# Performance work log

Measured on AMD Instinct MI355X. Metric: run time of the kernel, lower is better.

Reference implementation:

```python
import jax, jax.numpy as jnp
import numpy as np

B, T, D, L, K = 4, 2048, 2048, 2048, 4  # batch, seq, width, lru_width, conv temporal width


def setup_inputs() -> dict:
    key = jax.random.key(0)
    ks = jax.random.split(key, 12)
    s = 0.02
    f32 = jnp.float32
    return {
        "x": jax.random.normal(ks[0], (B, T, D), f32),
        "w_y": jax.random.normal(ks[1], (D, L), f32) * s,
        "b_y": jnp.zeros((L,), f32),
        "w_x": jax.random.normal(ks[2], (D, L), f32) * s,
        "b_x": jnp.zeros((L,), f32),
        "conv_w": jax.random.normal(ks[3], (K, L), f32) * s,
        "conv_b": jnp.zeros((L,), f32),
        "a_param": jax.random.uniform(ks[4], (L,), f32, 0.5, 4.0),
        "w_ig": jax.random.normal(ks[5], (L, L), f32) * s,
        "b_ig": jnp.zeros((L,), f32),
        "w_ag": jax.random.normal(ks[6], (L, L), f32) * s,
        "b_ag": jnp.zeros((L,), f32),
        "w_out": jax.random.normal(ks[7], (L, D), f32) * s,
        "b_out": jnp.zeros((D,), f32),
    }


def reference(x, w_y, b_y, w_x, b_x, conv_w, conv_b, a_param,
              w_ig, b_ig, w_ag, b_ag, w_out, b_out):
    # x: [B, T, D] (batch_first=True)
    Tn = x.shape[1]
    # gate branch: GELU(linear_y(x))
    y = jax.nn.gelu(jnp.einsum('btd,dl->btl', x, w_y) + b_y, approximate=False)
    # recurrent branch: linear_x -> causal depthwise conv1d (width K)
    xb = jnp.einsum('btd,dl->btl', x, w_x) + b_x
    xp = jnp.pad(xb, ((0, 0), (K - 1, 0), (0, 0)))  # zero left pad (fresh cache)
    conv = conv_b
    for k in range(K):  # y_t = b + sum_k w[k] * x_{t-(K-1-k)}
        conv = conv + conv_w[k] * xp[:, k:k + Tn]
    # RG-LRU
    gate_x = jax.nn.sigmoid(jnp.einsum('btl,lm->btm', conv, w_ig) + b_ig)
    gate_a = jax.nn.sigmoid(jnp.einsum('btl,lm->btm', conv, w_ag) + b_ag)
    log_a = -8.0 * gate_a * jax.nn.softplus(a_param)  # [B,T,L]
    a = jnp.exp(log_a)
    mult = jnp.sqrt(1.0 - jnp.exp(2.0 * log_a))
    reset = (jnp.arange(Tn) == 0)[None, :, None]  # reset at sequence start
    a = jnp.where(reset, 0.0, a)
    mult = jnp.where(reset, 1.0, mult)
    nx = gate_x * conv * mult
    # linear diagonal scan h_t = a_t * h_{t-1} + nx_t
    def step(h, inp):
        a_t, x_t = inp
        h = a_t * h + x_t
        return h, h
    h0 = jnp.zeros((x.shape[0], a.shape[-1]), x.dtype)
    hn, hs = jax.lax.scan(step, h0, (a.transpose(1, 0, 2), nx.transpose(1, 0, 2)))
    h_seq = hs.transpose(1, 0, 2)  # [B,T,L]
    out = jnp.einsum('btl,ld->btd', h_seq * y, w_out) + b_out
    return out, hn
```

## Files before the change

kernel.cpp:

```cpp
#include <hip/hip_runtime.h>
#include <math.h>

#define B_ 4
#define T_ 2048
#define D_ 2048
#define L_ 2048
#define KW 4
#define M_ (B_*T_)

typedef unsigned short u16;
typedef unsigned short u16x8 __attribute__((ext_vector_type(8)));
typedef __bf16 bf16x8 __attribute__((ext_vector_type(8)));
typedef float f32x4 __attribute__((ext_vector_type(4)));

__device__ __forceinline__ u16 f2bf(float f) {
    unsigned u = __float_as_uint(f);
    u += 0x7fffu + ((u >> 16) & 1u);
    return (u16)(u >> 16);
}
__device__ __forceinline__ float bf2f(u16 h) {
    return __uint_as_float(((unsigned)h) << 16);
}
__device__ __forceinline__ float gelu_exact(float v) {
    return 0.5f * v * (1.0f + erff(v * 0.70710678118654752440f));
}
__device__ __forceinline__ float sigmoidf_(float v) {
    return 1.0f / (1.0f + __expf(-v));
}
__device__ __forceinline__ void gload16(const void* g, void* l) {
    __builtin_amdgcn_global_load_lds(
        (const __attribute__((address_space(1))) void*)g,
        (__attribute__((address_space(3))) void*)l,
        16, 0, 0);
}
__device__ __forceinline__ void bar() {
    __builtin_amdgcn_s_barrier();
}

__global__ __launch_bounds__(256)
void castx_kernel(const float* __restrict__ in, u16* __restrict__ out)
{
    const int i = blockIdx.x * 256 + threadIdx.x;
    float4 v = ((const float4*)in)[i];
    ushort4 o;
    o.x = f2bf(v.x); o.y = f2bf(v.y); o.z = f2bf(v.z); o.w = f2bf(v.w);
    ((ushort4*)out)[i] = o;
}

__global__ __launch_bounds__(256)
void transcast_kernel(const float* __restrict__ in, u16* __restrict__ out,
                      int Kd, int Nd)
{
    __shared__ float tile[32][33];
    const int bx = blockIdx.x;
    const int by = blockIdx.y;
    const int tx = threadIdx.x & 31;
    const int ty = threadIdx.x >> 5;
    #pragma unroll
    for (int j = 0; j < 4; ++j) {
        const int r = by*32 + ty + j*8;
        tile[ty + j*8][tx] = in[(size_t)r * Nd + bx*32 + tx];
    }
    __syncthreads();
    #pragma unroll
    for (int j = 0; j < 4; ++j) {
        const int n = bx*32 + ty + j*8;
        out[(size_t)n * Kd + by*32 + tx] = f2bf(tile[tx][ty + j*8]);
    }
}

__device__ __forceinline__ void store_out(float* C, size_t idx, float v) { C[idx] = v; }
__device__ __forceinline__ void store_out(u16*   C, size_t idx, float v) { C[idx] = f2bf(v); }

template<int EPI, typename OutT>
__global__ __launch_bounds__(512)
void mgemm_kernel(const u16* __restrict__ A, const u16* __restrict__ BT,
                  const float* __restrict__ bias, OutT* __restrict__ C,
                  int M, int N, int K)
{
    __shared__ __align__(16) u16 lds[65536];
    u16* ldsA = lds;
    u16* ldsB = lds + 32768;

    const int tid  = threadIdx.x;
    const int wave = tid >> 6;
    const int lane = tid & 63;

    const int nbx = N >> 8;
    const int nwg = nbx * (M >> 8);
    const int bid = blockIdx.x;
    const int li  = (bid & 7) * (nwg >> 3) + (bid >> 3);
    const int bm  = (li / nbx) * 256;
    const int bn  = (li % nbx) * 256;

    const int wm = wave >> 2;
    const int wn = wave & 3;
    const int lr = lane & 15;
    const int q  = lane >> 4;
    const int sw = lane & 7;

    const int grow8 = lane >> 3;
    const int gslot = (lane & 7) ^ grow8;

    const int NT = K >> 6;

    const int c1 = (wave & 3) + (wave >> 2) * 8;
    const u16* gA0 = A  + (size_t)(bm + (wave     )*8 + grow8) * K + gslot*8;
    const u16* gA1 = A  + (size_t)(bm + (wave + 16)*8 + grow8) * K + gslot*8;
    const u16* gA2 = A  + (size_t)(bm + (wave +  8)*8 + grow8) * K + gslot*8;
    const u16* gA3 = A  + (size_t)(bm + (wave + 24)*8 + grow8) * K + gslot*8;
    const u16* gB0 = BT + (size_t)(bn + (c1       )*8 + grow8) * K + gslot*8;
    const u16* gB1 = BT + (size_t)(bn + (c1  + 16 )*8 + grow8) * K + gslot*8;
    const u16* gB2 = BT + (size_t)(bn + (c1  +  4 )*8 + grow8) * K + gslot*8;
    const u16* gB3 = BT + (size_t)(bn + (c1  + 20 )*8 + grow8) * K + gslot*8;
    const int dA0 = (wave     )*512 + lane*8, dA1 = (wave + 16)*512 + lane*8;
    const int dA2 = (wave +  8)*512 + lane*8, dA3 = (wave + 24)*512 + lane*8;
    const int dB0 = (c1       )*512 + lane*8, dB1 = (c1  + 16 )*512 + lane*8;
    const int dB2 = (c1  +  4 )*512 + lane*8, dB3 = (c1  + 20 )*512 + lane*8;

    auto ST_AH0 = [&](int g){ u16* b = ldsA + (g&1)*16384; const size_t kg = (size_t)g<<6;
        gload16(gA0+kg, &b[dA0]); gload16(gA1+kg, &b[dA1]); };
    auto ST_AH1 = [&](int g){ u16* b = ldsA + (g&1)*16384; const size_t kg = (size_t)g<<6;
        gload16(gA2+kg, &b[dA2]); gload16(gA3+kg, &b[dA3]); };
    auto ST_BH0 = [&](int g){ u16* b = ldsB + (g&1)*16384; const size_t kg = (size_t)g<<6;
        gload16(gB0+kg, &b[dB0]); gload16(gB1+kg, &b[dB1]); };
    auto ST_BH1 = [&](int g){ u16* b = ldsB + (g&1)*16384; const size_t kg = (size_t)g<<6;
        gload16(gB2+kg, &b[dB2]); gload16(gB3+kg, &b[dB3]); };

    const int ks0 = ((    q) ^ sw) * 8;
    const int ks1 = ((4 + q) ^ sw) * 8;

    auto LDA4 = [&](const u16* Ab, int half, bf16x8 (&dst)[4][2]) {
        #pragma unroll
        for (int i = 0; i < 4; ++i) {
            const int ro = (wm*128 + half*64 + i*16 + lr) * 64;
            dst[i][0] = *(const bf16x8*)&Ab[ro + ks0];
            dst[i][1] = *(const bf16x8*)&Ab[ro + ks1];
        }
    };
    auto LDB2 = [&](const u16* Bb, int half, bf16x8 (&dst)[2][2]) {
        #pragma unroll
        for (int j = 0; j < 2; ++j) {
            const int ro = (wn*64 + half*32 + j*16 + lr) * 64;
            dst[j][0] = *(const bf16x8*)&Bb[ro + ks0];
            dst[j][1] = *(const bf16x8*)&Bb[ro + ks1];
        }
    };

    f32x4 acc[8][4] = {};
    bf16x8 a0[4][2], a1[4][2], b0[2][2], b1[2][2];

    auto MM16 = [&](bf16x8 (&a)[4][2], bf16x8 (&b)[2][2], int mo, int no) {
        __builtin_amdgcn_s_setprio(1);
        #pragma unroll
        for (int ks = 0; ks < 2; ++ks)
            #pragma unroll
            for (int ii = 0; ii < 4; ++ii)
                #pragma unroll
                for (int jj = 0; jj < 2; ++jj)
                    acc[mo+ii][no+jj] = __builtin_amdgcn_mfma_f32_16x16x32_bf16(
                        a[ii][ks], b[jj][ks], acc[mo+ii][no+jj], 0, 0, 0);
        __builtin_amdgcn_s_setprio(0);
    };

    #define LGKM0() asm volatile("s_waitcnt lgkmcnt(0)" ::: "memory")

    ST_AH0(0); ST_BH0(0); ST_AH1(0); ST_BH1(0);
    ST_AH0(1); ST_BH0(1); ST_AH1(1); ST_BH1(1);
    asm volatile("s_waitcnt vmcnt(8)" ::: "memory");
    bar();

    for (int g = 0; g < NT; ++g) {
        const u16* Ab = ldsA + (g&1)*16384;
        const u16* Bb = ldsB + (g&1)*16384;
        const bool s1 = (g + 1 < NT), s2 = (g + 2 < NT);

        LDA4(Ab, 0, a0);
        LDB2(Bb, 0, b0);
        bar();
        LGKM0();
        MM16(a0, b0, 0, 0);
        bar();

        LDB2(Bb, 1, b1);
        if (s2) ST_AH0(g + 2);
        bar();
        LGKM0();
        MM16(a0, b1, 0, 2);
        bar();

        LDA4(Ab, 1, a1);
        if (s2) ST_BH0(g + 2);
        bar();
        LGKM0();
        MM16(a1, b1, 4, 2);
        bar();

        if (s2) { ST_AH1(g + 2); ST_BH1(g + 2); }
        bar();
        MM16(a1, b0, 4, 0);
        if (s2)      { asm volatile("s_waitcnt vmcnt(8)" ::: "memory"); }
        else if (s1) { asm volatile("s_waitcnt vmcnt(0)" ::: "memory"); }
        bar();
    }

    const int orow = (lane >> 4) * 4;
    float bv[4];
    #pragma unroll
    for (int nj = 0; nj < 4; ++nj) bv[nj] = bias[bn + wn*64 + nj*16 + lr];
    #pragma unroll
    for (int mi = 0; mi < 8; ++mi) {
        #pragma unroll
        for (int r = 0; r < 4; ++r) {
            const int row = bm + wm*128 + mi*16 + orow + r;
            const size_t rb = (size_t)row * N + bn + wn*64 + lr;
            #pragma unroll
            for (int nj = 0; nj < 4; ++nj) {
                float v = acc[mi][nj][r] + bv[nj];
                if (EPI == 1)      v = gelu_exact(v);
                else if (EPI == 2) v = sigmoidf_(v);
                store_out(C, rb + nj*16, v);
            }
        }
    }
    #undef LGKM0
}

__global__ __launch_bounds__(256)
void conv_kernel(const u16* __restrict__ xb, const float* __restrict__ cw,
                 const float* __restrict__ cb, u16* __restrict__ out)
{
    const int idx = blockIdx.x * 256 + threadIdx.x;
    const int NL8 = L_ / 8;
    const int l = (idx % NL8) * 8;
    const int bt = idx / NL8;
    const int t = bt & (T_ - 1);
    float acc[8];
    #pragma unroll
    for (int j = 0; j < 8; ++j) acc[j] = cb[l + j];
    #pragma unroll
    for (int k = 0; k < KW; ++k) {
        const int ts = t - (KW-1) + k;
        if (ts >= 0) {
            u16x8 xv = *(const u16x8*)(xb + ((size_t)(bt - (KW-1-k))) * L_ + l);
            #pragma unroll
            for (int j = 0; j < 8; ++j)
                acc[j] = fmaf(cw[k*L_ + l + j], bf2f(xv[j]), acc[j]);
        }
    }
    u16x8 o;
    #pragma unroll
    for (int j = 0; j < 8; ++j) o[j] = f2bf(acc[j]);
    *(u16x8*)(out + (size_t)bt * L_ + l) = o;
}

__global__ __launch_bounds__(256)
void rglru_kernel(const u16* __restrict__ conv, u16* __restrict__ gxa,
                  u16* __restrict__ ganx, const float* __restrict__ ap)
{
    const int idx = blockIdx.x * 256 + threadIdx.x;
    const int NL8 = L_ / 8;
    const int l = (idx % NL8) * 8;
    const int bt = idx / NL8;
    const int t = bt & (T_ - 1);
    const size_t off = (size_t)bt * L_ + l;
    u16x8 gx = *(u16x8*)(gxa + off);
    u16x8 ga = *(u16x8*)(ganx + off);
    u16x8 cv = *(const u16x8*)(conv + off);
    u16x8 av, nxv;
    #pragma unroll
    for (int j = 0; j < 8; ++j) {
        float p  = ap[l + j];
        float sp = log1pf(expf(p));
        float la = -8.0f * bf2f(ga[j]) * sp;
        float a  = expf(la);
        float mult = sqrtf(fmaxf(0.f, 1.0f - a*a));
        if (t == 0) { a = 0.f; mult = 1.f; }
        av[j]  = f2bf(a);
        nxv[j] = f2bf(bf2f(gx[j]) * bf2f(cv[j]) * mult);
    }
    *(u16x8*)(gxa + off)  = av;
    *(u16x8*)(ganx + off) = nxv;
}

#define CHUNKS 32
#define CLEN (T_ / CHUNKS)

__global__ __launch_bounds__(256)
void scan1_kernel(const u16* __restrict__ Ab, const u16* __restrict__ Xb,
                  float* __restrict__ Pb, float* __restrict__ Sb)
{
    const int l = blockIdx.x * 256 + threadIdx.x;
    const int c = blockIdx.y;
    const int b = blockIdx.z;
    size_t base = ((size_t)b * T_ + (size_t)c * CLEN) * L_ + l;
    float h = 0.f, P = 1.f;
    #pragma unroll 4
    for (int t = 0; t < CLEN; ++t) {
        float a = bf2f(Ab[base + (size_t)t * L_]);
        float x = bf2f(Xb[base + (size_t)t * L_]);
        h = fmaf(a, h, x);
        P *= a;
    }
    const size_t o = ((size_t)b * CHUNKS + c) * L_ + l;
    Pb[o] = P;
    Sb[o] = h;
}

__global__ __launch_bounds__(256)
void scan2_kernel(const float* __restrict__ Pb, const float* __restrict__ Sb,
                  float* __restrict__ Hin, float* __restrict__ hn)
{
    const int idx = blockIdx.x * 256 + threadIdx.x;
    const int l = idx & (L_ - 1);
    const int b = idx >> 11;
    float h = 0.f;
    for (int c = 0; c < CHUNKS; ++c) {
        const size_t o = ((size_t)b * CHUNKS + c) * L_ + l;
        Hin[o] = h;
        h = fmaf(Pb[o], h, Sb[o]);
    }
    hn[(size_t)b * L_ + l] = h;
}

__global__ __launch_bounds__(256)
void scan3_kernel(const u16* __restrict__ Ab, const u16* __restrict__ Xb,
                  const float* __restrict__ Hin, const u16* __restrict__ Yb,
                  u16* __restrict__ Zb)
{
    const int l = blockIdx.x * 256 + threadIdx.x;
    const int c = blockIdx.y;
    const int b = blockIdx.z;
    float h = Hin[((size_t)b * CHUNKS + c) * L_ + l];
    size_t base = ((size_t)b * T_ + (size_t)c * CLEN) * L_ + l;
    #pragma unroll 4
    for (int t = 0; t < CLEN; ++t) {
        const size_t o = base + (size_t)t * L_;
        h = fmaf(bf2f(Ab[o]), h, bf2f(Xb[o]));
        Zb[o] = f2bf(h * bf2f(Yb[o]));
    }
}

extern "C" void kernel_launch(void* const* d_in, const int* in_sizes, int n_in,
                              void* d_out, int out_size, void* d_ws, size_t ws_size,
                              hipStream_t stream)
{
    const float* x     = (const float*)d_in[0];
    const float* w_y   = (const float*)d_in[1];
    const float* b_y   = (const float*)d_in[2];
    const float* w_x   = (const float*)d_in[3];
    const float* b_x   = (const float*)d_in[4];
    const float* cw    = (const float*)d_in[5];
    const float* cb    = (const float*)d_in[6];
    const float* ap    = (const float*)d_in[7];
    const float* w_ig  = (const float*)d_in[8];
    const float* b_ig  = (const float*)d_in[9];
    const float* w_ag  = (const float*)d_in[10];
    const float* b_ag  = (const float*)d_in[11];
    const float* w_out = (const float*)d_in[12];
    const float* b_out = (const float*)d_in[13];

    float* out = (float*)d_out;
    float* hn  = out + (size_t)M_ * D_;

    const size_t MB = 1u << 20;
    char* w = (char*)d_ws;
    u16*  xbf   = (u16*)(w + 0);
    u16*  wigb  = (u16*)(w + 0);
    u16*  wagb  = (u16*)(w + 8*MB);
    u16*  zb    = (u16*)(w + 0);
    u16*  ybf   = (u16*)(w + 32*MB);
    u16*  xbbf  = (u16*)(w + 64*MB);
    u16*  woutb = (u16*)(w + 64*MB);
    float* Pb   = (float*)(w + 72*MB);
    float* Sb   = (float*)(w + 73*MB);
    float* Hin  = (float*)(w + 74*MB);
    u16*  wyb   = (u16*)(w + 96*MB);
    u16*  wxb   = (u16*)(w + 104*MB);
    u16*  convb = (u16*)(w + 96*MB);
    u16*  gx    = (u16*)(w + 128*MB);
    u16*  ga    = (u16*)(w + 160*MB);

    const dim3 blk(256);
    const dim3 blkG(512);
    const dim3 gG((L_/256) * (M_/256));
    const dim3 gT(2048/32, 2048/32);
    const int  gE8 = (M_ * L_ / 8) / 256;
    const dim3 gScan(L_/256, CHUNKS, B_);

    hipLaunchKernelGGL(castx_kernel, dim3((M_*D_/4)/256), blk, 0, stream, x, xbf);
    hipLaunchKernelGGL(transcast_kernel, gT, blk, 0, stream, w_y, wyb, D_, L_);
    hipLaunchKernelGGL(transcast_kernel, gT, blk, 0, stream, w_x, wxb, D_, L_);
    hipLaunchKernelGGL((mgemm_kernel<1, u16>), gG, blkG, 0, stream, xbf, wyb, b_y, ybf, M_, L_, D_);
    hipLaunchKernelGGL((mgemm_kernel<0, u16>), gG, blkG, 0, stream, xbf, wxb, b_x, xbbf, M_, L_, D_);
    hipLaunchKernelGGL(transcast_kernel, gT, blk, 0, stream, w_ig, wigb, L_, L_);
    hipLaunchKernelGGL(transcast_kernel, gT, blk, 0, stream, w_ag, wagb, L_, L_);
    hipLaunchKernelGGL(conv_kernel, dim3(gE8), blk, 0, stream, xbbf, cw, cb, convb);
    hipLaunchKernelGGL(transcast_kernel, gT, blk, 0, stream, w_out, woutb, L_, D_);
    hipLaunchKernelGGL((mgemm_kernel<2, u16>), gG, blkG, 0, stream, convb, wigb, b_ig, gx, M_, L_, L_);
    hipLaunchKernelGGL((mgemm_kernel<2, u16>), gG, blkG, 0, stream, convb, wagb, b_ag, ga, M_, L_, L_);
    hipLaunchKernelGGL(rglru_kernel, dim3(gE8), blk, 0, stream, convb, gx, ga, ap);
    hipLaunchKernelGGL(scan1_kernel, gScan, blk, 0, stream, gx, ga, Pb, Sb);
    hipLaunchKernelGGL(scan2_kernel, dim3(B_*L_/256), blk, 0, stream, Pb, Sb, Hin, hn);
    hipLaunchKernelGGL(scan3_kernel, gScan, blk, 0, stream, gx, ga, Hin, ybf, zb);
    hipLaunchKernelGGL((mgemm_kernel<0, float>), gG, blkG, 0, stream, zb, woutb, b_out, out, M_, D_, L_);
}
```

Before: 544.6 us.

## Software-pipeline LDS fragment loads across k-tiles with partial lgkmcnt waits

Restructures the GEMM main loop so LDS-to-register fragment loads for the next k-tile (A half 0 and B half 0) are issued during the current tile's MFMAs, using ping-pong B registers and an unroll by two. Full lgkmcnt(0) waits and several barriers are replaced with partial lgkmcnt/vmcnt waits, so LDS reads and global prefetch overlap with matrix math. This costs extra registers and relies on the wait counts matching the number of outstanding operations. It also assumes NT is even.

Result: slower. 1.615 ms (+196.5%).

```diff
diff --git a/kernel.cpp b/kernel.cpp
--- a/kernel.cpp
+++ b/kernel.cpp
@@ -148,7 +148,7 @@
     };
 
     f32x4 acc[8][4] = {};
-    bf16x8 a0[4][2], a1[4][2], b0[2][2], b1[2][2];
+    bf16x8 a0[4][2], a1[4][2], b0p[2][2], b0q[2][2], b1[2][2];
 
     auto MM16 = [&](bf16x8 (&a)[4][2], bf16x8 (&b)[2][2], int mo, int no) {
         __builtin_amdgcn_s_setprio(1);
@@ -163,45 +163,54 @@
         __builtin_amdgcn_s_setprio(0);
     };
 
-    #define LGKM0() asm volatile("s_waitcnt lgkmcnt(0)" ::: "memory")
-
     ST_AH0(0); ST_BH0(0); ST_AH1(0); ST_BH1(0);
     ST_AH0(1); ST_BH0(1); ST_AH1(1); ST_BH1(1);
     asm volatile("s_waitcnt vmcnt(8)" ::: "memory");
     bar();
-
-    for (int g = 0; g < NT; ++g) {
-        const u16* Ab = ldsA + (g&1)*16384;
-        const u16* Bb = ldsB + (g&1)*16384;
+    LDB2(ldsB, 0, b0p);
+    LDA4(ldsA, 0, a0);
+
+    auto ktile = [&](int g, bf16x8 (&b0cur)[2][2], bf16x8 (&b0nxt)[2][2]) {
+        const u16* Ab  = ldsA + (g&1)*16384;
+        const u16* Bb  = ldsB + (g&1)*16384;
+        const u16* AbN = ldsA + ((g+1)&1)*16384;
+        const u16* BbN = ldsB + ((g+1)&1)*16384;
         const bool s1 = (g + 1 < NT), s2 = (g + 2 < NT);
 
-        LDA4(Ab, 0, a0);
-        LDB2(Bb, 0, b0);
+        LDB2(Bb, 1, b1);
+        asm volatile("s_waitcnt lgkmcnt(4)" ::: "memory");
+        MM16(a0, b0cur, 0, 0);
         bar();
-        LGKM0();
-        MM16(a0, b0, 0, 0);
+
+        LDA4(Ab, 1, a1);
+        if (s2) ST_AH0(g + 2);
+        asm volatile("s_waitcnt lgkmcnt(8)" ::: "memory");
+        MM16(a0, b1, 0, 2);
+        if (s2)      { asm volatile("s_waitcnt vmcnt(2)" ::: "memory"); }
+        else if (s1) { asm volatile("s_waitcnt vmcnt(0)" ::: "memory"); }
         bar();
 
-        LDB2(Bb, 1, b1);
-        if (s2) ST_AH0(g + 2);
-        bar();
-        LGKM0();
-        MM16(a0, b1, 0, 2);
-        bar();
-
-        LDA4(Ab, 1, a1);
-        if (s2) ST_BH0(g + 2);
-        bar();
-        LGKM0();
+        if (s1) {
+            LDB2(BbN, 0, b0nxt);
+            if (s2) ST_BH0(g + 2);
+            asm volatile("s_waitcnt lgkmcnt(4)" ::: "memory");
+        } else {
+            asm volatile("s_waitcnt lgkmcnt(0)" ::: "memory");
+        }
         MM16(a1, b1, 4, 2);
         bar();
 
-        if (s2) { ST_AH1(g + 2); ST_BH1(g + 2); }
+        if (s1) {
+            LDA4(AbN, 0, a0);
+            if (s2) { ST_AH1(g + 2); ST_BH1(g + 2); }
+        }
+        MM16(a1, b0cur, 4, 0);
         bar();
-        MM16(a1, b0, 4, 0);
-        if (s2)      { asm volatile("s_waitcnt vmcnt(8)" ::: "memory"); }
-        else if (s1) { asm volatile("s_waitcnt vmcnt(0)" ::: "memory"); }
-        bar();
+    };
+
+    for (int g = 0; g < NT; g += 2) {
+        ktile(g,     b0p, b0q);
+        ktile(g + 1, b0q, b0p);
     }
 
     const int orow = (lane >> 4) * 4;
@@ -223,7 +232,6 @@
             }
         }
     }
-    #undef LGKM0
 }
 
 __global__ __launch_bounds__(256)
```
